# Performance work log

Hardware: AMD Instinct MI355X
Metric: run time of the kernel (lower is better)

The kernel has to match this reference:

```python
import jax, jax.numpy as jnp
import numpy as np
from jax import lax

D, H_HEADS, DEPTH, E, HID, P, NCLS = 768, 12, 12, 4, 3072, 16, 1000

def _ln(x, w, b, eps=1e-5):
    m = x.mean(-1, keepdims=True)
    v = ((x - m) ** 2).mean(-1, keepdims=True)
    return (x - m) * lax.rsqrt(v + eps) * w + b

def setup_inputs() -> dict:
    key = jax.random.key(0)
    ks = jax.random.split(key, 16)
    s = 0.02
    inp = {
        'x': jax.random.normal(ks[0], (32, 3, 224, 224), jnp.float32),
        'conv_w': jax.random.normal(ks[1], (D, 3, P, P), jnp.float32) * s,
        'conv_b': jnp.zeros((D,), jnp.float32),
        'cls_token': jnp.zeros((1, 1, D), jnp.float32),
        'pos_embed': jax.random.normal(ks[2], (1, 197, D), jnp.float32) * s,
        'ln1_w': jnp.ones((DEPTH, D), jnp.float32),
        'ln1_b': jnp.zeros((DEPTH, D), jnp.float32),
        'qkv_w': jax.random.normal(ks[3], (DEPTH, 3 * D, D), jnp.float32) * s,
        'qkv_b': jnp.zeros((DEPTH, 3 * D), jnp.float32),
        'out_w': jax.random.normal(ks[4], (DEPTH, D, D), jnp.float32) * s,
        'out_b': jnp.zeros((DEPTH, D), jnp.float32),
        'ln2_w': jnp.ones((DEPTH, D), jnp.float32),
        'ln2_b': jnp.zeros((DEPTH, D), jnp.float32),
        'gate_w': jax.random.normal(ks[5], (DEPTH, E, D), jnp.float32) * s,
        'gate_b': jnp.zeros((DEPTH, E), jnp.float32),
        'e1_w': jax.random.normal(ks[6], (DEPTH, E, HID, D), jnp.float32) * s,
        'e1_b': jnp.zeros((DEPTH, E, HID), jnp.float32),
        'e2_w': jax.random.normal(ks[7], (DEPTH, E, D, HID), jnp.float32) * s,
        'e2_b': jnp.zeros((DEPTH, E, D), jnp.float32),
        'fnorm_w': jnp.ones((D,), jnp.float32),
        'fnorm_b': jnp.zeros((D,), jnp.float32),
        'head_w': jax.random.normal(ks[8], (NCLS, D), jnp.float32) * s,
        'head_b': jnp.zeros((NCLS,), jnp.float32),
    }
    return inp

def reference(x, conv_w, conv_b, cls_token, pos_embed, ln1_w, ln1_b, qkv_w, qkv_b,
              out_w, out_b, ln2_w, ln2_b, gate_w, gate_b, e1_w, e1_b, e2_w, e2_b,
              fnorm_w, fnorm_b, head_w, head_b):
    B = x.shape[0]
    # patch embedding: conv stride=patch, then flatten -> [B, N, D]
    x = lax.conv_general_dilated(x, conv_w, (P, P), 'VALID',
                                 dimension_numbers=('NCHW', 'OIHW', 'NCHW'))
    x = x + conv_b[None, :, None, None]
    x = x.reshape(B, D, -1).transpose(0, 2, 1)
    x = jnp.concatenate([jnp.broadcast_to(cls_token, (B, 1, D)), x], axis=1)
    x = x + pos_embed
    N = x.shape[1]
    hd = D // H_HEADS
    for i in range(DEPTH):
        # --- attention ---
        h = x
        y = _ln(x, ln1_w[i], ln1_b[i])
        qkv = y @ qkv_w[i].T + qkv_b[i]                      # [B,N,3D]
        q, k, v = jnp.split(qkv, 3, axis=-1)
        q = q.reshape(B, N, H_HEADS, hd).transpose(0, 2, 1, 3) / jnp.sqrt(hd).astype(x.dtype)
        k = k.reshape(B, N, H_HEADS, hd).transpose(0, 2, 1, 3)
        v = v.reshape(B, N, H_HEADS, hd).transpose(0, 2, 1, 3)
        attn = jax.nn.softmax(jnp.einsum('bhqd,bhkd->bhqk', q, k), axis=-1)
        ctx = jnp.einsum('bhqk,bhkd->bhqd', attn, v).transpose(0, 2, 1, 3).reshape(B, N, D)
        x = h + (ctx @ out_w[i].T + out_b[i])
        # --- MoE MLP (dense: all experts computed then masked, top_k=1) ---
        h = x
        y = _ln(x, ln2_w[i], ln2_b[i])
        gate = y @ gate_w[i].T + gate_b[i]                   # [B,N,E]
        topk_scores, topk_idx = lax.top_k(gate, 1)           # [B,N,1]
        score = jax.nn.softmax(topk_scores, axis=-1)[..., 0]  # [B,N] (==1 for k=1)
        h1 = jax.nn.gelu(jnp.einsum('bnd,ehd->benh', y, e1_w[i])
                         + e1_b[i][None, :, None, :], approximate=False)  # [B,E,N,HID]
        oe = jnp.einsum('benh,edh->bend', h1, e2_w[i]) + e2_b[i][None, :, None, :]
        mask = jax.nn.one_hot(topk_idx[..., 0], E, dtype=y.dtype)  # [B,N,E]
        moe = jnp.einsum('bne,bend->bnd', mask * score[..., None], oe)
        x = h + moe
    x = _ln(x, fnorm_w, fnorm_b)
    cls = x[:, 0]
    return cls @ head_w.T + head_b
```

## Files before the change

kernel.cpp:

```cpp
#include <hip/hip_runtime.h>
#include <hip/hip_bf16.h>
#include <math.h>

#define D_MODEL 768
#define SEQ     197
#define BATCH   32
#define NTOK    (BATCH*SEQ)
#define NHEAD   12
#define HDIM    64
#define NEXP    4
#define HID_N   3072
#define DEPTH_N 12

typedef __attribute__((ext_vector_type(4))) float f32x4;
typedef __attribute__((ext_vector_type(8))) short bf16x8;
typedef __attribute__((ext_vector_type(4))) unsigned short u16x4;
typedef unsigned short u16;

static __device__ __forceinline__ u16 f2bf(float f){
  unsigned int u = __builtin_bit_cast(unsigned int, f);
  u += 0x7FFFu + ((u >> 16) & 1u);
  return (u16)(u >> 16);
}
static __device__ __forceinline__ void split_bf(float x, u16& h, u16& l){
  h = f2bf(x);
  float hf = __builtin_bit_cast(float, (unsigned)h << 16);
  l = f2bf(x - hf);
}

static __device__ __forceinline__ float wred_sum(float v){
  #pragma unroll
  for (int off = 32; off; off >>= 1) v += __shfl_down(v, off);
  return v;
}

static __device__ __forceinline__ void gld16(const u16* g, u16* l){
  __builtin_amdgcn_global_load_lds(
      (const __attribute__((address_space(1))) unsigned int*)g,
      (__attribute__((address_space(3))) unsigned int*)l, 16, 0, 0);
}

__global__ __launch_bounds__(256) void split_many(const float* __restrict__ src,
                                                  u16* __restrict__ hi,
                                                  u16* __restrict__ lo, long n4){
  for (long i = blockIdx.x*256L + threadIdx.x; i < n4; i += (long)gridDim.x*256){
    f32x4 v = *reinterpret_cast<const f32x4*>(src + i*4);
    u16x4 h, l;
    #pragma unroll
    for (int j = 0; j < 4; j++){ u16 hh, ll; split_bf(v[j], hh, ll); h[j]=hh; l[j]=ll; }
    *reinterpret_cast<u16x4*>(hi + i*4) = h;
    *reinterpret_cast<u16x4*>(lo + i*4) = l;
  }
}

template<int MODE, int NG>
__global__ __launch_bounds__(256, 2) void gemm_split(
    const u16* __restrict__ Ahp, const u16* __restrict__ Alp,
    const u16* __restrict__ Whp, const u16* __restrict__ Wlp,
    const float* __restrict__ bias, const float* __restrict__ resid,
    float* __restrict__ C, const float* __restrict__ pos,
    u16* __restrict__ Chi, u16* __restrict__ Clo,
    const int* __restrict__ toks, const int* __restrict__ cnts,
    const int* __restrict__ offs, const int* __restrict__ tiles,
    int MTg, int NBg, int M, int N, int K)
{
  const int tid = threadIdx.x;
  const int NB = N >> 7;
  const int xcd = blockIdx.x & 7;
  const int idx = blockIdx.x >> 3;
  const int mg = xcd / NG, ng = xcd - mg*NG;
  const int mt = mg*MTg + idx / NBg;
  const int nb = ng*NBg + idx % NBg;
  if (nb >= NB) return;

  int cnt = M, base = 0, m0;
  if (MODE == 2 || MODE == 3){
    if (mt >= tiles[0]) return;
    const int e = tiles[1 + 2*mt];
    m0 = tiles[2 + 2*mt];
    cnt  = cnts[e];
    base = offs[e];
    Whp  += (size_t)e * N * K;
    Wlp  += (size_t)e * N * K;
    bias += (size_t)e * N;
  } else {
    m0 = mt * 128;
    if (m0 >= M) return;
  }
  const int n0 = nb * 128;

  __shared__ __align__(16) u16 lds[2][4][4096];

  const int lane = tid & 63, wid = tid >> 6;
  const int i0 = wid*128 + lane;
  const int r0 = i0 >> 2, r1 = r0 + 16;
  const int x0 = (i0 & 3) ^ ((r0 >> 1) & 3);
  const int x1 = (i0 & 3) ^ ((r1 >> 1) & 3);
  const int d0 = wid*1024, d1 = wid*1024 + 512;

  size_t aA0 = 0, aA1 = 0, pb0 = 0, pb1 = 0;
  {
    const int gm0 = m0 + r0, gm1 = m0 + r1;
    if (MODE == 0 || MODE == 1){
      aA0 = (size_t)(gm0 < M ? gm0 : 0) * K + x0*8;
      aA1 = (size_t)(gm1 < M ? gm1 : 0) * K + x1*8;
    }
    if (MODE == 2){
      aA0 = (size_t)(gm0 < cnt ? toks[base+gm0] : 0) * K + x0*8;
      aA1 = (size_t)(gm1 < cnt ? toks[base+gm1] : 0) * K + x1*8;
    }
    if (MODE == 3){
      aA0 = (size_t)(gm0 < cnt ? base+gm0 : 0) * K + x0*8;
      aA1 = (size_t)(gm1 < cnt ? base+gm1 : 0) * K + x1*8;
    }
    if (MODE == 4){
      int b_ = gm0 / 196, pp = gm0 - b_*196;
      pb0 = (size_t)b_*150528 + (size_t)(pp/14)*3584 + (size_t)(pp%14)*16;
      b_ = gm1 / 196; pp = gm1 - b_*196;
      pb1 = (size_t)b_*150528 + (size_t)(pp/14)*3584 + (size_t)(pp%14)*16;
    }
  }
  const size_t aW0 = (size_t)(n0 + r0) * K + x0*8;
  const size_t aW1 = (size_t)(n0 + r1) * K + x1*8;

  auto STAGE = [&](int buf, int t){
    const int k0 = t * 32;
    if (MODE == 4){
      const int kq0 = k0 + x0*8, kq1 = k0 + x1*8;
      size_t a0 = pb0 + (size_t)(kq0>>8)*50176 + (size_t)((kq0>>4)&15)*224 + (size_t)(kq0&15);
      size_t a1 = pb1 + (size_t)(kq1>>8)*50176 + (size_t)((kq1>>4)&15)*224 + (size_t)(kq1&15);
      gld16(Ahp + a0, &lds[buf][0][d0]); gld16(Ahp + a1, &lds[buf][0][d1]);
      gld16(Alp + a0, &lds[buf][1][d0]); gld16(Alp + a1, &lds[buf][1][d1]);
    } else {
      gld16(Ahp + aA0 + k0, &lds[buf][0][d0]); gld16(Ahp + aA1 + k0, &lds[buf][0][d1]);
      gld16(Alp + aA0 + k0, &lds[buf][1][d0]); gld16(Alp + aA1 + k0, &lds[buf][1][d1]);
    }
    gld16(Whp + aW0 + k0, &lds[buf][2][d0]); gld16(Whp + aW1 + k0, &lds[buf][2][d1]);
    gld16(Wlp + aW0 + k0, &lds[buf][3][d0]); gld16(Wlp + aW1 + k0, &lds[buf][3][d1]);
  };

  const int wr = wid >> 1, wc = wid & 1;
  const int lr = lane & 15, lq = lane >> 4;
  int cA[4], cW[4];
  #pragma unroll
  for (int mi = 0; mi < 4; mi++){
    int ra = wr*64 + mi*16 + lr;
    cA[mi] = (4*ra + (lq ^ ((ra>>1)&3))) * 8;
  }
  #pragma unroll
  for (int nj = 0; nj < 4; nj++){
    int rw = wc*64 + nj*16 + lr;
    cW[nj] = (4*rw + (lq ^ ((rw>>1)&3))) * 8;
  }

  const int NT = K >> 5;
  f32x4 acc[4][4] = {};

  STAGE(0, 0);
  for (int t = 0; t < NT; t++){
    const int buf = t & 1;
    if (t + 1 < NT){
      STAGE(buf ^ 1, t + 1);
      asm volatile("s_waitcnt vmcnt(8)" ::: "memory");
    } else {
      asm volatile("s_waitcnt vmcnt(0)" ::: "memory");
    }
    __builtin_amdgcn_s_barrier();
    asm volatile("" ::: "memory");
    const u16* L = &lds[buf][0][0];
    bf16x8 afh[4], afl[4], bfh[4], bfl[4];
    #pragma unroll
    for (int mi = 0; mi < 4; mi++){
      afh[mi] = *reinterpret_cast<const bf16x8*>(L + cA[mi]);
      afl[mi] = *reinterpret_cast<const bf16x8*>(L + 4096 + cA[mi]);
    }
    #pragma unroll
    for (int nj = 0; nj < 4; nj++){
      bfh[nj] = *reinterpret_cast<const bf16x8*>(L + 2*4096 + cW[nj]);
      bfl[nj] = *reinterpret_cast<const bf16x8*>(L + 3*4096 + cW[nj]);
    }
    #pragma unroll
    for (int mi = 0; mi < 4; mi++)
      #pragma unroll
      for (int nj = 0; nj < 4; nj++){
        acc[mi][nj] = __builtin_amdgcn_mfma_f32_16x16x32_bf16(afh[mi], bfh[nj], acc[mi][nj], 0, 0, 0);
        acc[mi][nj] = __builtin_amdgcn_mfma_f32_16x16x32_bf16(afh[mi], bfl[nj], acc[mi][nj], 0, 0, 0);
        acc[mi][nj] = __builtin_amdgcn_mfma_f32_16x16x32_bf16(afl[mi], bfh[nj], acc[mi][nj], 0, 0, 0);
      }
    asm volatile("" ::: "memory");
    __builtin_amdgcn_s_barrier();
  }

  #pragma unroll
  for (int nj = 0; nj < 4; nj++){
    const int ncol = n0 + wc*64 + nj*16 + lr;
    const float bv = bias[ncol];
    #pragma unroll
    for (int mi = 0; mi < 4; mi++){
      const int mb = m0 + wr*64 + mi*16 + lq*4;
      #pragma unroll
      for (int j = 0; j < 4; j++){
        const int m = mb + j;
        float v = acc[mi][nj][j] + bv;
        if (MODE == 0){
          if (m < M) C[(size_t)m * N + ncol] = v;
        }
        if (MODE == 1){
          if (m < M) C[(size_t)m * N + ncol] = v + resid[(size_t)m * N + ncol];
        }
        if (MODE == 2){
          if (m < cnt){
            v = 0.5f * v * (1.f + erff(v * 0.70710678118f));
            u16 h, l; split_bf(v, h, l);
            Chi[(size_t)(base + m) * N + ncol] = h;
            Clo[(size_t)(base + m) * N + ncol] = l;
          }
        }
        if (MODE == 3){
          if (m < cnt){
            int tok = toks[base + m];
            C[(size_t)tok * N + ncol] += v;
          }
        }
        if (MODE == 4){
          int b_ = m / 196, pp = m - b_ * 196;
          C[((size_t)b_ * 197 + 1 + pp) * D_MODEL + ncol] =
              v + pos[(size_t)(1 + pp) * D_MODEL + ncol];
        }
      }
    }
  }
}

__global__ __launch_bounds__(256) void cls_init(const float* __restrict__ cls_tk,
                                                const float* __restrict__ pos,
                                                float* __restrict__ xt){
  const int b = blockIdx.x, tid = threadIdx.x;
  for (int d = tid; d < D_MODEL; d += 256)
    xt[((size_t)b*SEQ)*D_MODEL + d] = cls_tk[d] + pos[d];
}

__global__ __launch_bounds__(256) void ln_kernel(const float* __restrict__ x, size_t xstride,
                                                 const float* __restrict__ w,
                                                 const float* __restrict__ b,
                                                 float* __restrict__ y, size_t ystride,
                                                 u16* __restrict__ yh, u16* __restrict__ yl){
  const int t = blockIdx.x;
  const int tid = threadIdx.x;
  const float* row = x + (size_t)t*xstride;
  float v0 = row[tid], v1 = row[tid+256], v2 = row[tid+512];
  __shared__ float red[4];
  float s = wred_sum(v0+v1+v2);
  if ((tid & 63) == 0) red[tid>>6] = s;
  __syncthreads();
  const float mean = (red[0]+red[1]+red[2]+red[3]) * (1.f/768.f);
  const float d0 = v0-mean, d1 = v1-mean, d2 = v2-mean;
  __syncthreads();
  float q = wred_sum(d0*d0 + d1*d1 + d2*d2);
  if ((tid & 63) == 0) red[tid>>6] = q;
  __syncthreads();
  const float var = (red[0]+red[1]+red[2]+red[3]) * (1.f/768.f);
  const float inv = rsqrtf(var + 1e-5f);
  float o0 = d0*inv*w[tid]     + b[tid];
  float o1 = d1*inv*w[tid+256] + b[tid+256];
  float o2 = d2*inv*w[tid+512] + b[tid+512];
  float* yr = y + (size_t)t*ystride;
  yr[tid] = o0; yr[tid+256] = o1; yr[tid+512] = o2;
  if (yh){
    u16 h, l;
    size_t rb = (size_t)t*768;
    split_bf(o0, h, l); yh[rb+tid]     = h; yl[rb+tid]     = l;
    split_bf(o1, h, l); yh[rb+tid+256] = h; yl[rb+tid+256] = l;
    split_bf(o2, h, l); yh[rb+tid+512] = h; yl[rb+tid+512] = l;
  }
}

__global__ __launch_bounds__(256, 3) void attn_f32(const float* __restrict__ qkv,
                                                   u16* __restrict__ ctxh,
                                                   u16* __restrict__ ctxl){
  const int qt = blockIdx.x, h = blockIdx.y, b = blockIdx.z;
  const int tid = threadIdx.x;
  const int tx = tid & 15, ty = tid >> 4;
  __shared__ float Qs[64][65];
  __shared__ float KPs[64][65];
  __shared__ float Vs[64][65];
  const size_t rs = 3*D_MODEL;
  const float* base = qkv + (size_t)b*SEQ*rs + (size_t)h*HDIM;

  #pragma unroll
  for (int it = 0; it < 16; it++){
    int idx = tid + it*256;
    int r = idx >> 6, c = idx & 63;
    int gq = qt*64 + r;
    float v = (gq < SEQ) ? base[(size_t)gq*rs + c] : 0.f;
    Qs[r][c] = v * 0.125f;
  }
  float m_run[4], l_run[4], o[4][4];
  #pragma unroll
  for (int i = 0; i < 4; i++){
    m_run[i] = -3.0e38f; l_run[i] = 0.f;
    #pragma unroll
    for (int j = 0; j < 4; j++) o[i][j] = 0.f;
  }
  __syncthreads();

  for (int kt = 0; kt < 4; kt++){
    #pragma unroll
    for (int it = 0; it < 16; it++){
      int idx = tid + it*256;
      int r = idx >> 6, c = idx & 63;
      int gk = kt*64 + r;
      float kv = (gk < SEQ) ? base[(size_t)gk*rs + D_MODEL   + c] : 0.f;
      float vv = (gk < SEQ) ? base[(size_t)gk*rs + 2*D_MODEL + c] : 0.f;
      KPs[r][c] = kv;
      Vs[r][c]  = vv;
    }
    __syncthreads();
    float s[4][4] = {};
    for (int d = 0; d < 64; d++){
      float qv[4], kv2[4];
      #pragma unroll
      for (int i = 0; i < 4; i++) qv[i]  = Qs[ty*4+i][d];
      #pragma unroll
      for (int j = 0; j < 4; j++) kv2[j] = KPs[tx*4+j][d];
      #pragma unroll
      for (int i = 0; i < 4; i++)
        #pragma unroll
        for (int j = 0; j < 4; j++) s[i][j] += qv[i]*kv2[j];
    }
    #pragma unroll
    for (int j = 0; j < 4; j++){
      if (kt*64 + tx*4 + j >= SEQ){
        #pragma unroll
        for (int i = 0; i < 4; i++) s[i][j] = -3.0e38f;
      }
    }
    float scale[4];
    #pragma unroll
    for (int i = 0; i < 4; i++){
      float mt = fmaxf(fmaxf(s[i][0], s[i][1]), fmaxf(s[i][2], s[i][3]));
      #pragma unroll
      for (int msk = 1; msk <= 8; msk <<= 1) mt = fmaxf(mt, __shfl_xor(mt, msk));
      float mnew = fmaxf(m_run[i], mt);
      scale[i] = __expf(m_run[i] - mnew);
      float ls = 0.f;
      #pragma unroll
      for (int j = 0; j < 4; j++){ s[i][j] = __expf(s[i][j] - mnew); ls += s[i][j]; }
      #pragma unroll
      for (int msk = 1; msk <= 8; msk <<= 1) ls += __shfl_xor(ls, msk);
      l_run[i] = l_run[i]*scale[i] + ls;
      m_run[i] = mnew;
    }
    __syncthreads();
    #pragma unroll
    for (int i = 0; i < 4; i++)
      #pragma unroll
      for (int j = 0; j < 4; j++) KPs[ty*4+i][tx*4+j] = s[i][j];
    __syncthreads();
    #pragma unroll
    for (int i = 0; i < 4; i++)
      #pragma unroll
      for (int j = 0; j < 4; j++) o[i][j] *= scale[i];
    for (int k = 0; k < 64; k++){
      float pv[4], vv[4];
      #pragma unroll
      for (int i = 0; i < 4; i++) pv[i] = KPs[ty*4+i][k];
      #pragma unroll
      for (int j = 0; j < 4; j++) vv[j] = Vs[k][tx*4+j];
      #pragma unroll
      for (int i = 0; i < 4; i++)
        #pragma unroll
        for (int j = 0; j < 4; j++) o[i][j] += pv[i]*vv[j];
    }
    __syncthreads();
  }
  #pragma unroll
  for (int i = 0; i < 4; i++){
    int q = qt*64 + ty*4 + i;
    if (q < SEQ){
      float inv = 1.f / l_run[i];
      #pragma unroll
      for (int j = 0; j < 4; j++){
        u16 hh, ll;
        split_bf(o[i][j]*inv, hh, ll);
        size_t idx = ((size_t)(b*SEQ + q))*D_MODEL + h*HDIM + tx*4 + j;
        ctxh[idx] = hh; ctxl[idx] = ll;
      }
    }
  }
}

__global__ __launch_bounds__(256) void gate_kernel(const float* __restrict__ y,
                                                   const float* __restrict__ gw,
                                                   const float* __restrict__ gb,
                                                   int* __restrict__ eidx,
                                                   int* __restrict__ counts){
  const int t = blockIdx.x;
  const int tid = threadIdx.x;
  const int e = tid >> 6, lane = tid & 63;
  const float* row = y + (size_t)t*D_MODEL;
  const float* wrow = gw + (size_t)e*D_MODEL;
  float acc = 0.f;
  for (int k = lane; k < D_MODEL; k += 64) acc += row[k]*wrow[k];
  acc = wred_sum(acc);
  __shared__ float sc[NEXP];
  if (lane == 0) sc[e] = acc + gb[e];
  __syncthreads();
  if (tid == 0){
    int best = 0; float bv = sc[0];
    #pragma unroll
    for (int k = 1; k < NEXP; k++) if (sc[k] > bv){ bv = sc[k]; best = k; }
    eidx[t] = best;
    atomicAdd(&counts[best], 1);
  }
}

__global__ void zero_counts(int* c){ if (threadIdx.x < 3*NEXP) c[threadIdx.x] = 0; }

__global__ void offsets_kernel(const int* counts, int* offs, int* cursor, int* tiles){
  if (threadIdx.x == 0){
    int o = 0, n = 0;
    for (int e = 0; e < NEXP; e++){
      offs[e] = o; cursor[e] = o;
      for (int m0 = 0; m0 < counts[e]; m0 += 128){
        tiles[1+2*n] = e; tiles[2+2*n] = m0; n++;
      }
      o += counts[e];
    }
    tiles[0] = n;
  }
}

__global__ __launch_bounds__(256) void scatter_kernel(const int* __restrict__ eidx,
                                                      int* cursor, int* __restrict__ toks){
  int i = blockIdx.x*256 + threadIdx.x;
  if (i < NTOK){ int pos = atomicAdd(&cursor[eidx[i]], 1); toks[pos] = i; }
}

__global__ __launch_bounds__(256) void gemm_f32(const float* __restrict__ A,
                                                const float* __restrict__ W,
                                                const float* __restrict__ bias,
                                                const float* __restrict__ resid,
                                                float* __restrict__ C,
                                                int M, int N, int K){
  const int m0 = blockIdx.x*64, bn = blockIdx.y*64;
  const int tid = threadIdx.x;
  const int tx = tid & 15, ty = tid >> 4;
  __shared__ float As[16][65];
  __shared__ float Ws[16][65];
  float acc[4][4] = {};
  for (int k0 = 0; k0 < K; k0 += 16){
    #pragma unroll
    for (int i = 0; i < 4; i++){
      int idx = tid + i*256;
      int k = idx & 15, m = idx >> 4;
      As[k][m] = (m0+m < M) ? A[(size_t)(m0+m)*K + k0 + k] : 0.f;
      Ws[k][m] = (bn+m < N) ? W[(size_t)(bn+m)*K + k0 + k] : 0.f;
    }
    __syncthreads();
    #pragma unroll
    for (int kk = 0; kk < 16; kk++){
      float a0 = As[kk][ty*4+0], a1 = As[kk][ty*4+1], a2 = As[kk][ty*4+2], a3 = As[kk][ty*4+3];
      float w0 = Ws[kk][tx*4+0], w1 = Ws[kk][tx*4+1], w2 = Ws[kk][tx*4+2], w3 = Ws[kk][tx*4+3];
      acc[0][0] += a0*w0; acc[0][1] += a0*w1; acc[0][2] += a0*w2; acc[0][3] += a0*w3;
      acc[1][0] += a1*w0; acc[1][1] += a1*w1; acc[1][2] += a1*w2; acc[1][3] += a1*w3;
      acc[2][0] += a2*w0; acc[2][1] += a2*w1; acc[2][2] += a2*w2; acc[2][3] += a2*w3;
      acc[3][0] += a3*w0; acc[3][1] += a3*w1; acc[3][2] += a3*w2; acc[3][3] += a3*w3;
    }
    __syncthreads();
  }
  #pragma unroll
  for (int i = 0; i < 4; i++){
    int m = m0 + ty*4 + i;
    if (m >= M) continue;
    #pragma unroll
    for (int j = 0; j < 4; j++){
      int n = bn + tx*4 + j;
      if (n >= N) continue;
      float v = acc[i][j];
      if (bias)  v += bias[n];
      if (resid) v += resid[(size_t)m*N + n];
      C[(size_t)m*N + n] = v;
    }
  }
}

extern "C" void kernel_launch(void* const* d_in, const int* in_sizes, int n_in,
                              void* d_out, int out_size, void* d_ws, size_t ws_size,
                              hipStream_t stream){
  const float* x      = (const float*)d_in[0];
  const float* conv_w = (const float*)d_in[1];
  const float* conv_b = (const float*)d_in[2];
  const float* cls_tk = (const float*)d_in[3];
  const float* pos    = (const float*)d_in[4];
  const float* ln1w   = (const float*)d_in[5];
  const float* ln1b   = (const float*)d_in[6];
  const float* qkvw   = (const float*)d_in[7];
  const float* qkvb   = (const float*)d_in[8];
  const float* outw   = (const float*)d_in[9];
  const float* outb   = (const float*)d_in[10];
  const float* ln2w   = (const float*)d_in[11];
  const float* ln2b   = (const float*)d_in[12];
  const float* gatew  = (const float*)d_in[13];
  const float* gateb  = (const float*)d_in[14];
  const float* e1w    = (const float*)d_in[15];
  const float* e1b    = (const float*)d_in[16];
  const float* e2w    = (const float*)d_in[17];
  const float* e2b    = (const float*)d_in[18];
  const float* fnw    = (const float*)d_in[19];
  const float* fnb    = (const float*)d_in[20];
  const float* headw  = (const float*)d_in[21];
  const float* headb  = (const float*)d_in[22];
  float* out = (float*)d_out;

  float* ws    = (float*)d_ws;
  float* xt    = ws;
  float* y     = xt  + (size_t)NTOK*D_MODEL;
  float* qkv   = y   + (size_t)NTOK*D_MODEL;
  float* clsln = qkv + (size_t)NTOK*3*D_MODEL;
  int*   eidx   = (int*)(clsln + (size_t)BATCH*D_MODEL);
  int*   toks   = eidx + NTOK;
  int*   counts = toks + NTOK;
  int*   offs   = counts + NEXP;
  int*   cursor = offs + NEXP;
  int*   tiles  = cursor + NEXP;
  u16* up = (u16*)(((size_t)(tiles + 120) + 15) & ~(size_t)15);
  const size_t nY  = (size_t)NTOK*D_MODEL;
  const size_t nH1 = (size_t)NTOK*HID_N;
  const size_t nX  = (size_t)BATCH*3*224*224;
  const size_t nCW = 768*768;
  const size_t nQW = (size_t)DEPTH_N*3*D_MODEL*D_MODEL;
  const size_t nOW = (size_t)DEPTH_N*D_MODEL*D_MODEL;
  const size_t nE1 = (size_t)DEPTH_N*NEXP*HID_N*D_MODEL;
  const size_t nE2 = (size_t)DEPTH_N*NEXP*D_MODEL*HID_N;
  u16 *yh = up,      *yl = yh + nY;
  u16 *ch = yl + nY, *cl = ch + nY;
  u16 *h1h = cl + nY, *h1l = h1h + nH1;
  u16 *xh = h1l + nH1, *xl = xh + nX;
  u16 *cwh = xl + nX,  *cwl = cwh + nCW;
  u16 *qwh = cwl + nCW, *qwl = qwh + nQW;
  u16 *owh = qwl + nQW, *owl = owh + nOW;
  u16 *e1h = owl + nOW, *e1l = e1h + nE1;
  u16 *e2h = e1l + nE1, *e2l = e2h + nE2;

  dim3 b256(256);

  split_many<<<2048, b256, 0, stream>>>(x,      xh,  xl,  (long)(nX/4));
  split_many<<<2048, b256, 0, stream>>>(conv_w, cwh, cwl, (long)(nCW/4));
  split_many<<<2048, b256, 0, stream>>>(qkvw,   qwh, qwl, (long)(nQW/4));
  split_many<<<2048, b256, 0, stream>>>(outw,   owh, owl, (long)(nOW/4));
  split_many<<<2048, b256, 0, stream>>>(e1w,    e1h, e1l, (long)(nE1/4));
  split_many<<<2048, b256, 0, stream>>>(e2w,    e2h, e2l, (long)(nE2/4));

  gemm_split<4,2><<<dim3(8*13*3), b256, 0, stream>>>(xh, xl, cwh, cwl,
      conv_b, nullptr, xt, pos, nullptr, nullptr,
      nullptr, nullptr, nullptr, nullptr, 13, 3, 6272, D_MODEL, 768);
  cls_init<<<dim3(BATCH), b256, 0, stream>>>(cls_tk, pos, xt);

  for (int i = 0; i < DEPTH_N; i++){
    ln_kernel<<<dim3(NTOK), b256, 0, stream>>>(xt, D_MODEL,
        ln1w + (size_t)i*D_MODEL, ln1b + (size_t)i*D_MODEL, y, D_MODEL, yh, yl);
    gemm_split<0,2><<<dim3(8*13*9), b256, 0, stream>>>(yh, yl,
        qwh + (size_t)i*3*D_MODEL*D_MODEL, qwl + (size_t)i*3*D_MODEL*D_MODEL,
        qkvb + (size_t)i*3*D_MODEL, nullptr, qkv, nullptr, nullptr, nullptr,
        nullptr, nullptr, nullptr, nullptr, 13, 9, NTOK, 3*D_MODEL, D_MODEL);
    attn_f32<<<dim3(4, NHEAD, BATCH), b256, 0, stream>>>(qkv, ch, cl);
    gemm_split<1,2><<<dim3(8*13*3), b256, 0, stream>>>(ch, cl,
        owh + (size_t)i*D_MODEL*D_MODEL, owl + (size_t)i*D_MODEL*D_MODEL,
        outb + (size_t)i*D_MODEL, xt, xt, nullptr, nullptr, nullptr,
        nullptr, nullptr, nullptr, nullptr, 13, 3, NTOK, D_MODEL, D_MODEL);
    ln_kernel<<<dim3(NTOK), b256, 0, stream>>>(xt, D_MODEL,
        ln2w + (size_t)i*D_MODEL, ln2b + (size_t)i*D_MODEL, y, D_MODEL, yh, yl);
    zero_counts<<<1, 64, 0, stream>>>(counts);
    gate_kernel<<<dim3(NTOK), b256, 0, stream>>>(y,
        gatew + (size_t)i*NEXP*D_MODEL, gateb + (size_t)i*NEXP, eidx, counts);
    offsets_kernel<<<1, 64, 0, stream>>>(counts, offs, cursor, tiles);
    scatter_kernel<<<dim3((NTOK+255)/256), b256, 0, stream>>>(eidx, cursor, toks);
    gemm_split<2,4><<<dim3(8*27*6), b256, 0, stream>>>(yh, yl,
        e1h + (size_t)i*NEXP*HID_N*D_MODEL, e1l + (size_t)i*NEXP*HID_N*D_MODEL,
        e1b + (size_t)i*NEXP*HID_N, nullptr, nullptr, nullptr, h1h, h1l,
        toks, counts, offs, tiles, 27, 6, NTOK, HID_N, D_MODEL);
    gemm_split<3,2><<<dim3(8*14*3), b256, 0, stream>>>(h1h, h1l,
        e2h + (size_t)i*NEXP*D_MODEL*HID_N, e2l + (size_t)i*NEXP*D_MODEL*HID_N,
        e2b + (size_t)i*NEXP*D_MODEL, nullptr, xt, nullptr, nullptr, nullptr,
        toks, counts, offs, tiles, 14, 3, NTOK, D_MODEL, HID_N);
  }

  ln_kernel<<<dim3(BATCH), b256, 0, stream>>>(xt, (size_t)SEQ*D_MODEL, fnw, fnb,
      clsln, D_MODEL, nullptr, nullptr);
  gemm_f32<<<dim3(1, 16), b256, 0, stream>>>(clsln, headw, headb, nullptr, out, BATCH, 1000, D_MODEL);
}
```

Measured before the change: 10.62 ms.

## Add 256x256-tile 512-thread split-bf16 GEMM for QKV and expert-up projections

Introduces a larger-tile GEMM kernel (256x256 output per block, 512 threads, 8x4 MFMA accumulators per wave) and uses it for the QKV projection and the first expert GEMM with fused GELU. Larger tiles raise arithmetic intensity and cut operand reloads from global memory and LDS per MFMA. The offsets kernel now builds both 128- and 256-row expert tile lists. The counts zeroing is folded into the LN kernel, and the unused fp32 LN output is skipped before QKV. The trade-off is one block per CU with more registers, and more padding waste on the expert tiles.

```diff
diff --git a/kernel.cpp b/kernel.cpp
--- a/kernel.cpp
+++ b/kernel.cpp
@@ -59,7 +59,6 @@
     const u16* __restrict__ Whp, const u16* __restrict__ Wlp,
     const float* __restrict__ bias, const float* __restrict__ resid,
     float* __restrict__ C, const float* __restrict__ pos,
-    u16* __restrict__ Chi, u16* __restrict__ Clo,
     const int* __restrict__ toks, const int* __restrict__ cnts,
     const int* __restrict__ offs, const int* __restrict__ tiles,
     int MTg, int NBg, int M, int N, int K)
@@ -74,7 +73,7 @@
   if (nb >= NB) return;
 
   int cnt = M, base = 0, m0;
-  if (MODE == 2 || MODE == 3){
+  if (MODE == 3){
     if (mt >= tiles[0]) return;
     const int e = tiles[1 + 2*mt];
     m0 = tiles[2 + 2*mt];
@@ -101,13 +100,9 @@
   size_t aA0 = 0, aA1 = 0, pb0 = 0, pb1 = 0;
   {
     const int gm0 = m0 + r0, gm1 = m0 + r1;
-    if (MODE == 0 || MODE == 1){
+    if (MODE == 1){
       aA0 = (size_t)(gm0 < M ? gm0 : 0) * K + x0*8;
       aA1 = (size_t)(gm1 < M ? gm1 : 0) * K + x1*8;
-    }
-    if (MODE == 2){
-      aA0 = (size_t)(gm0 < cnt ? toks[base+gm0] : 0) * K + x0*8;
-      aA1 = (size_t)(gm1 < cnt ? toks[base+gm1] : 0) * K + x1*8;
     }
     if (MODE == 3){
       aA0 = (size_t)(gm0 < cnt ? base+gm0 : 0) * K + x0*8;
@@ -202,19 +197,8 @@
       for (int j = 0; j < 4; j++){
         const int m = mb + j;
         float v = acc[mi][nj][j] + bv;
-        if (MODE == 0){
-          if (m < M) C[(size_t)m * N + ncol] = v;
-        }
         if (MODE == 1){
           if (m < M) C[(size_t)m * N + ncol] = v + resid[(size_t)m * N + ncol];
-        }
-        if (MODE == 2){
-          if (m < cnt){
-            v = 0.5f * v * (1.f + erff(v * 0.70710678118f));
-            u16 h, l; split_bf(v, h, l);
-            Chi[(size_t)(base + m) * N + ncol] = h;
-            Clo[(size_t)(base + m) * N + ncol] = l;
-          }
         }
         if (MODE == 3){
           if (m < cnt){
@@ -232,6 +216,149 @@
   }
 }
 
+template<int MODE, int NG>
+__global__ __launch_bounds__(512, 1) void gemm_split_big(
+    const u16* __restrict__ Ahp, const u16* __restrict__ Alp,
+    const u16* __restrict__ Whp, const u16* __restrict__ Wlp,
+    const float* __restrict__ bias, float* __restrict__ C,
+    u16* __restrict__ Chi, u16* __restrict__ Clo,
+    const int* __restrict__ toks, const int* __restrict__ cnts,
+    const int* __restrict__ offs, const int* __restrict__ tiles,
+    int MTg, int NBg, int M, int N, int K)
+{
+  const int tid = threadIdx.x;
+  const int NB = N >> 8;
+  const int xcd = blockIdx.x & 7;
+  const int idx = blockIdx.x >> 3;
+  const int mg = xcd / NG, ng = xcd - mg*NG;
+  const int mt = mg*MTg + idx / NBg;
+  const int nb = ng*NBg + idx % NBg;
+  if (nb >= NB) return;
+
+  int cnt = M, base = 0, m0;
+  if (MODE == 2){
+    if (mt >= tiles[0]) return;
+    const int e = tiles[1 + 2*mt];
+    m0 = tiles[2 + 2*mt];
+    cnt  = cnts[e];
+    base = offs[e];
+    Whp  += (size_t)e * N * K;
+    Wlp  += (size_t)e * N * K;
+    bias += (size_t)e * N;
+  } else {
+    m0 = mt * 256;
+    if (m0 >= M) return;
+  }
+  const int n0 = nb * 256;
+
+  __shared__ __align__(16) u16 Alds[2][2][8192];
+  __shared__ __align__(16) u16 Wlds[2][2][8192];
+
+  const int lane = tid & 63, wid = tid >> 6;
+  const int i0 = wid*128 + lane;
+  const int r0 = i0 >> 2, r1 = r0 + 16;
+  const int x0 = (i0 & 3) ^ ((r0 >> 1) & 3);
+  const int x1 = (i0 & 3) ^ ((r1 >> 1) & 3);
+  const int d0 = wid*1024, d1 = wid*1024 + 512;
+
+  size_t aA0, aA1;
+  {
+    const int gm0 = m0 + r0, gm1 = m0 + r1;
+    if (MODE == 0){
+      aA0 = (size_t)(gm0 < M ? gm0 : 0) * K + x0*8;
+      aA1 = (size_t)(gm1 < M ? gm1 : 0) * K + x1*8;
+    } else {
+      aA0 = (size_t)(gm0 < cnt ? toks[base+gm0] : 0) * K + x0*8;
+      aA1 = (size_t)(gm1 < cnt ? toks[base+gm1] : 0) * K + x1*8;
+    }
+  }
+  const size_t aW0 = (size_t)(n0 + r0) * K + x0*8;
+  const size_t aW1 = (size_t)(n0 + r1) * K + x1*8;
+
+  auto STAGE = [&](int buf, int t){
+    const int k0 = t * 32;
+    gld16(Ahp + aA0 + k0, &Alds[buf][0][d0]); gld16(Ahp + aA1 + k0, &Alds[buf][0][d1]);
+    gld16(Alp + aA0 + k0, &Alds[buf][1][d0]); gld16(Alp + aA1 + k0, &Alds[buf][1][d1]);
+    gld16(Whp + aW0 + k0, &Wlds[buf][0][d0]); gld16(Whp + aW1 + k0, &Wlds[buf][0][d1]);
+    gld16(Wlp + aW0 + k0, &Wlds[buf][1][d0]); gld16(Wlp + aW1 + k0, &Wlds[buf][1][d1]);
+  };
+
+  const int wr = wid >> 2, wcN = wid & 3;
+  const int lr = lane & 15, lq = lane >> 4;
+  int cA[8], cW[4];
+  #pragma unroll
+  for (int mi = 0; mi < 8; mi++){
+    int ra = wr*128 + mi*16 + lr;
+    cA[mi] = (4*ra + (lq ^ ((ra>>1)&3))) * 8;
+  }
+  #pragma unroll
+  for (int nj = 0; nj < 4; nj++){
+    int rw = wcN*64 + nj*16 + lr;
+    cW[nj] = (4*rw + (lq ^ ((rw>>1)&3))) * 8;
+  }
+
+  const int NT = K >> 5;
+  f32x4 acc[8][4] = {};
+
+  STAGE(0, 0);
+  for (int t = 0; t < NT; t++){
+    const int buf = t & 1;
+    if (t + 1 < NT){
+      STAGE(buf ^ 1, t + 1);
+      asm volatile("s_waitcnt vmcnt(8)" ::: "memory");
+    } else {
+      asm volatile("s_waitcnt vmcnt(0)" ::: "memory");
+    }
+    __builtin_amdgcn_s_barrier();
+    asm volatile("" ::: "memory");
+    bf16x8 bfh[4], bfl[4];
+    #pragma unroll
+    for (int nj = 0; nj < 4; nj++){
+      bfh[nj] = *reinterpret_cast<const bf16x8*>(&Wlds[buf][0][cW[nj]]);
+      bfl[nj] = *reinterpret_cast<const bf16x8*>(&Wlds[buf][1][cW[nj]]);
+    }
+    #pragma unroll
+    for (int mi = 0; mi < 8; mi++){
+      bf16x8 afh = *reinterpret_cast<const bf16x8*>(&Alds[buf][0][cA[mi]]);
+      bf16x8 afl = *reinterpret_cast<const bf16x8*>(&Alds[buf][1][cA[mi]]);
+      #pragma unroll
+      for (int nj = 0; nj < 4; nj++){
+        acc[mi][nj] = __builtin_amdgcn_mfma_f32_16x16x32_bf16(afh, bfh[nj], acc[mi][nj], 0, 0, 0);
+        acc[mi][nj] = __builtin_amdgcn_mfma_f32_16x16x32_bf16(afh, bfl[nj], acc[mi][nj], 0, 0, 0);
+        acc[mi][nj] = __builtin_amdgcn_mfma_f32_16x16x32_bf16(afl, bfh[nj], acc[mi][nj], 0, 0, 0);
+      }
+    }
+    asm volatile("" ::: "memory");
+    __builtin_amdgcn_s_barrier();
+  }
+
+  #pragma unroll
+  for (int nj = 0; nj < 4; nj++){
+    const int ncol = n0 + wcN*64 + nj*16 + lr;
+    const float bv = bias[ncol];
+    #pragma unroll
+    for (int mi = 0; mi < 8; mi++){
+      const int mb = m0 + wr*128 + mi*16 + lq*4;
+      #pragma unroll
+      for (int j = 0; j < 4; j++){
+        const int m = mb + j;
+        float v = acc[mi][nj][j] + bv;
+        if (MODE == 0){
+          if (m < M) C[(size_t)m * N + ncol] = v;
+        }
+        if (MODE == 2){
+          if (m < cnt){
+            v = 0.5f * v * (1.f + erff(v * 0.70710678118f));
+            u16 h, l; split_bf(v, h, l);
+            Chi[(size_t)(base + m) * N + ncol] = h;
+            Clo[(size_t)(base + m) * N + ncol] = l;
+          }
+        }
+      }
+    }
+  }
+}
+
 __global__ __launch_bounds__(256) void cls_init(const float* __restrict__ cls_tk,
                                                 const float* __restrict__ pos,
                                                 float* __restrict__ xt){
@@ -244,9 +371,11 @@
                                                  const float* __restrict__ w,
                                                  const float* __restrict__ b,
                                                  float* __restrict__ y, size_t ystride,
-                                                 u16* __restrict__ yh, u16* __restrict__ yl){
+                                                 u16* __restrict__ yh, u16* __restrict__ yl,
+                                                 int* __restrict__ zero4){
   const int t = blockIdx.x;
   const int tid = threadIdx.x;
+  if (zero4 && t == 0 && tid < NEXP) zero4[tid] = 0;
   const float* row = x + (size_t)t*xstride;
   float v0 = row[tid], v1 = row[tid+256], v2 = row[tid+512];
   __shared__ float red[4];
@@ -264,8 +393,10 @@
   float o0 = d0*inv*w[tid]     + b[tid];
   float o1 = d1*inv*w[tid+256] + b[tid+256];
   float o2 = d2*inv*w[tid+512] + b[tid+512];
-  float* yr = y + (size_t)t*ystride;
-  yr[tid] = o0; yr[tid+256] = o1; yr[tid+512] = o2;
+  if (y){
+    float* yr = y + (size_t)t*ystride;
+    yr[tid] = o0; yr[tid+256] = o1; yr[tid+512] = o2;
+  }
   if (yh){
     u16 h, l;
     size_t rb = (size_t)t*768;
@@ -415,19 +546,21 @@
   }
 }
 
-__global__ void zero_counts(int* c){ if (threadIdx.x < 3*NEXP) c[threadIdx.x] = 0; }
-
-__global__ void offsets_kernel(const int* counts, int* offs, int* cursor, int* tiles){
+__global__ void offsets_kernel(const int* counts, int* offs, int* cursor,
+                               int* t128, int* t256){
   if (threadIdx.x == 0){
-    int o = 0, n = 0;
+    int o = 0, n1 = 0, n2 = 0;
     for (int e = 0; e < NEXP; e++){
       offs[e] = o; cursor[e] = o;
       for (int m0 = 0; m0 < counts[e]; m0 += 128){
-        tiles[1+2*n] = e; tiles[2+2*n] = m0; n++;
+        t128[1+2*n1] = e; t128[2+2*n1] = m0; n1++;
+      }
+      for (int m0 = 0; m0 < counts[e]; m0 += 256){
+        t256[1+2*n2] = e; t256[2+2*n2] = m0; n2++;
       }
       o += counts[e];
     }
-    tiles[0] = n;
+    t128[0] = n1; t256[0] = n2;
   }
 }
 
@@ -518,13 +651,14 @@
   float* y     = xt  + (size_t)NTOK*D_MODEL;
   float* qkv   = y   + (size_t)NTOK*D_MODEL;
   float* clsln = qkv + (size_t)NTOK*3*D_MODEL;
-  int*   eidx   = (int*)(clsln + (size_t)BATCH*D_MODEL);
-  int*   toks   = eidx + NTOK;
-  int*   counts = toks + NTOK;
-  int*   offs   = counts + NEXP;
-  int*   cursor = offs + NEXP;
-  int*   tiles  = cursor + NEXP;
-  u16* up = (u16*)(((size_t)(tiles + 120) + 15) & ~(size_t)15);
+  int*   eidx    = (int*)(clsln + (size_t)BATCH*D_MODEL);
+  int*   toks    = eidx + NTOK;
+  int*   counts  = toks + NTOK;
+  int*   offs    = counts + NEXP;
+  int*   cursor  = offs + NEXP;
+  int*   tiles128 = cursor + NEXP;
+  int*   tiles256 = tiles128 + 128;
+  u16* up = (u16*)(((size_t)(tiles256 + 80) + 15) & ~(size_t)15);
   const size_t nY  = (size_t)NTOK*D_MODEL;
   const size_t nH1 = (size_t)NTOK*HID_N;
   const size_t nX  = (size_t)BATCH*3*224*224;
@@ -543,7 +677,7 @@
   u16 *e1h = owl + nOW, *e1l = e1h + nE1;
   u16 *e2h = e1l + nE1, *e2l = e2h + nE2;
 
-  dim3 b256(256);
+  dim3 b256(256), b512(512);
 
   split_many<<<2048, b256, 0, stream>>>(x,      xh,  xl,  (long)(nX/4));
   split_many<<<2048, b256, 0, stream>>>(conv_w, cwh, cwl, (long)(nCW/4));
@@ -553,40 +687,42 @@
   split_many<<<2048, b256, 0, stream>>>(e2w,    e2h, e2l, (long)(nE2/4));
 
   gemm_split<4,2><<<dim3(8*13*3), b256, 0, stream>>>(xh, xl, cwh, cwl,
-      conv_b, nullptr, xt, pos, nullptr, nullptr,
-      nullptr, nullptr, nullptr, nullptr, 13, 3, 6272, D_MODEL, 768);
+      conv_b, nullptr, xt, pos, nullptr, nullptr, nullptr, nullptr,
+      13, 3, 6272, D_MODEL, 768);
   cls_init<<<dim3(BATCH), b256, 0, stream>>>(cls_tk, pos, xt);
 
   for (int i = 0; i < DEPTH_N; i++){
     ln_kernel<<<dim3(NTOK), b256, 0, stream>>>(xt, D_MODEL,
-        ln1w + (size_t)i*D_MODEL, ln1b + (size_t)i*D_MODEL, y, D_MODEL, yh, yl);
-    gemm_split<0,2><<<dim3(8*13*9), b256, 0, stream>>>(yh, yl,
+        ln1w + (size_t)i*D_MODEL, ln1b + (size_t)i*D_MODEL,
+        nullptr, D_MODEL, yh, yl, nullptr);
+    gemm_split_big<0,2><<<dim3(8*7*5), b512, 0, stream>>>(yh, yl,
         qwh + (size_t)i*3*D_MODEL*D_MODEL, qwl + (size_t)i*3*D_MODEL*D_MODEL,
-        qkvb + (size_t)i*3*D_MODEL, nullptr, qkv, nullptr, nullptr, nullptr,
-        nullptr, nullptr, nullptr, nullptr, 13, 9, NTOK, 3*D_MODEL, D_MODEL);
+        qkvb + (size_t)i*3*D_MODEL, qkv, nullptr, nullptr,
+        nullptr, nullptr, nullptr, nullptr, 7, 5, NTOK, 3*D_MODEL, D_MODEL);
     attn_f32<<<dim3(4, NHEAD, BATCH), b256, 0, stream>>>(qkv, ch, cl);
     gemm_split<1,2><<<dim3(8*13*3), b256, 0, stream>>>(ch, cl,
         owh + (size_t)i*D_MODEL*D_MODEL, owl + (size_t)i*D_MODEL*D_MODEL,
-        outb + (size_t)i*D_MODEL, xt, xt, nullptr, nullptr, nullptr,
-        nullptr, nullptr, nullptr, nullptr, 13, 3, NTOK, D_MODEL, D_MODEL);
+        outb + (size_t)i*D_MODEL, xt, xt, nullptr,
+        nullptr, nullptr, nullptr, nullptr,
+        13, 3, NTOK, D_MODEL, D_MODEL);
     ln_kernel<<<dim3(NTOK), b256, 0, stream>>>(xt, D_MODEL,
-        ln2w + (size_t)i*D_MODEL, ln2b + (size_t)i*D_MODEL, y, D_MODEL, yh, yl);
-    zero_counts<<<1, 64, 0, stream>>>(counts);
+        ln2w + (size_t)i*D_MODEL, ln2b + (size_t)i*D_MODEL,
+        y, D_MODEL, yh, yl, counts);
     gate_kernel<<<dim3(NTOK), b256, 0, stream>>>(y,
         gatew + (size_t)i*NEXP*D_MODEL, gateb + (size_t)i*NEXP, eidx, counts);
-    offsets_kernel<<<1, 64, 0, stream>>>(counts, offs, cursor, tiles);
+    offsets_kernel<<<1, 64, 0, stream>>>(counts, offs, cursor, tiles128, tiles256);
     scatter_kernel<<<dim3((NTOK+255)/256), b256, 0, stream>>>(eidx, cursor, toks);
-    gemm_split<2,4><<<dim3(8*27*6), b256, 0, stream>>>(yh, yl,
+    gemm_split_big<2,4><<<dim3(8*14*3), b512, 0, stream>>>(yh, yl,
         e1h + (size_t)i*NEXP*HID_N*D_MODEL, e1l + (size_t)i*NEXP*HID_N*D_MODEL,
-        e1b + (size_t)i*NEXP*HID_N, nullptr, nullptr, nullptr, h1h, h1l,
-        toks, counts, offs, tiles, 27, 6, NTOK, HID_N, D_MODEL);
+        e1b + (size_t)i*NEXP*HID_N, nullptr, h1h, h1l,
+        toks, counts, offs, tiles256, 14, 3, NTOK, HID_N, D_MODEL);
     gemm_split<3,2><<<dim3(8*14*3), b256, 0, stream>>>(h1h, h1l,
         e2h + (size_t)i*NEXP*D_MODEL*HID_N, e2l + (size_t)i*NEXP*D_MODEL*HID_N,
-        e2b + (size_t)i*NEXP*D_MODEL, nullptr, xt, nullptr, nullptr, nullptr,
-        toks, counts, offs, tiles, 14, 3, NTOK, D_MODEL, HID_N);
+        e2b + (size_t)i*NEXP*D_MODEL, nullptr, xt, nullptr,
+        toks, counts, offs, tiles128, 14, 3, NTOK, D_MODEL, HID_N);
   }
 
   ln_kernel<<<dim3(BATCH), b256, 0, stream>>>(xt, (size_t)SEQ*D_MODEL, fnw, fnb,
-      clsln, D_MODEL, nullptr, nullptr);
+      clsln, D_MODEL, nullptr, nullptr, nullptr);
   gemm_f32<<<dim3(1, 16), b256, 0, stream>>>(clsln, headw, headb, nullptr, out, BATCH, 1000, D_MODEL);
 }
```

Result: slower. 12.84 ms (+20.9%).
